# Kernel tuning notes

Measured on AMD Instinct MI355X. Metric: run time of the kernel, lower is better.

## Reference

```python
import jax, jax.numpy as jnp
import numpy as np

MIN_, MAX_, KSZ, IGNORE_IDX = 10, 10, 3, -255
B, H, W = 256, 256, 256
LI_MAX_ITERS = 64


def setup_inputs() -> dict:
    key = jax.random.key(0)
    x = jax.random.uniform(key, (B, 1, H, W), dtype=jnp.float32)
    return {"x": x}


def _otsu(hist):
    # hist: [256] counts. Returns Otsu threshold (bin value); fg = img > t.
    bins = jnp.arange(256, dtype=jnp.float32)
    w0 = jnp.cumsum(hist)[:-1]
    w1 = hist.sum() - w0
    s0 = jnp.cumsum(hist * bins)[:-1]
    s_tot = (hist * bins).sum()
    m0 = s0 / jnp.maximum(w0, 1e-12)
    m1 = (s_tot - s0) / jnp.maximum(w1, 1e-12)
    var_b = w0 * w1 * (m0 - m1) ** 2
    return jnp.argmax(var_b).astype(jnp.float32)


def _li(hist, init_t):
    # Histogram-based Li iterative minimum cross-entropy threshold
    # (skimage.filters.threshold_li with initial_guess=init_t).
    bins = jnp.arange(256, dtype=jnp.float32)
    img_min = jnp.min(jnp.where(hist > 0, bins, 255.0))
    vals = bins - img_min  # shift so values >= 0 (as skimage does)
    csum = jnp.cumsum(hist)
    cvsum = jnp.cumsum(hist * vals)
    n_tot, s_tot = csum[-1], cvsum[-1]
    tol = 0.5  # integer image -> half the minimal value spacing

    def body(state):
        t_curr, _, i = state
        # background: img <= t_curr + img_min
        idx = jnp.clip(jnp.floor(t_curr + img_min).astype(jnp.int32), 0, 255)
        n_back, s_back = csum[idx], cvsum[idx]
        n_fore, s_fore = n_tot - n_back, s_tot - s_back
        mean_back = jnp.where(n_back > 0, s_back / jnp.maximum(n_back, 1.0), 0.0)
        mean_fore = s_fore / jnp.maximum(n_fore, 1.0)
        eps = 1e-12
        t_next = (mean_back - mean_fore) / (
            jnp.log(jnp.maximum(mean_back, eps)) - jnp.log(jnp.maximum(mean_fore, eps)))
        t_next = jnp.where(mean_back < eps, mean_fore / 2.0, t_next)
        return (t_next, t_curr, i + 1)

    def cond(state):
        t_curr, t_prev, i = state
        return (jnp.abs(t_curr - t_prev) > tol) & (i < LI_MAX_ITERS)

    t0 = init_t - img_min
    t_fin, _, _ = jax.lax.while_loop(cond, body, (t0, t0 + 10.0, 0))
    return t_fin + img_min


def _sample_mask(key, region, k):
    # Uniform sampling without replacement of up to k pixels from region
    # (bool [H,W]) via random-score top-k (equiv. to torch.multinomial
    # with uniform probs, w/o replacement).
    flat = region.reshape(-1)
    scores = jnp.where(flat, jax.random.uniform(key, (flat.shape[0],)), -1.0)
    top, idx = jax.lax.top_k(scores, k)
    valid = (top >= 0.0).astype(jnp.int32)
    mask = jnp.zeros(flat.shape[0], jnp.int32).at[idx].max(valid)
    return mask.reshape(region.shape)


def _dilate(m):
    # kornia dilation with ones (KSZ,KSZ) kernel on a 0/1 mask == max filter.
    return jax.lax.reduce_window(m, 0, jax.lax.max, (KSZ, KSZ), (1, 1), "SAME")


def _per_image(img_u8, key_fg, key_bg):
    # img_u8: [H,W] int32 in [0,255]
    hist = jnp.zeros(256, jnp.float32).at[img_u8.ravel()].add(1.0)
    otsu = jnp.clip(_otsu(hist), 1.0, 254.0)  # clamp 0->1, 255->254
    li_t = _li(hist, otsu)
    roi = img_u8.astype(jnp.float32) > li_t

    fg = _sample_mask(key_fg, roi, MAX_)
    bg = _sample_mask(key_bg, jnp.logical_not(roi), MIN_)
    if KSZ > 1:
        fg = _dilate(fg)
        bg = _dilate(bg)

    overlap = (fg + bg) == 2
    fg = jnp.where(overlap, 0, fg)
    bg = jnp.where(overlap, 0, bg)

    seeds = jnp.full((H, W), IGNORE_IDX, jnp.int32)
    seeds = jnp.where(bg == 1, 0, seeds)
    seeds = jnp.where(fg == 1, 1, seeds)
    return seeds


def reference(x):
    b = x.shape[0]
    # (cam*255).astype(uint8): truncation, cam in [0,1]
    img = jnp.clip(jnp.floor(x[:, 0] * 255.0), 0, 255).astype(jnp.int32)
    keys = jax.random.split(jax.random.key(1), (b, 2))
    return jax.vmap(_per_image)(img, keys[:, 0], keys[:, 1])
```

## Files before the change

### kernel.cpp

```cpp
#include <hip/hip_runtime.h>
#include <stdint.h>

#define NPIX 65536
#define IGN (-255)
#define CAP 1022
#define U8N    16384
#define HPART  16384
#define M_THR  18432
#define M_CF   18433
#define M_CB   18434
#define M_NROI 18435
#define M_FG   18436
#define M_BG   19458
#define SCR_I4 5120

__device__ __forceinline__ uint32_t rotl32(uint32_t v, uint32_t r){ return (v<<r)|(v>>(32u-r)); }

__device__ __forceinline__ void tf2x32(uint32_t k0, uint32_t k1, uint32_t x0, uint32_t x1,
                                       uint32_t &o0, uint32_t &o1){
  uint32_t k2 = k0 ^ k1 ^ 0x1BD11BDAu;
  x0 += k0; x1 += k1;
#define TFR(r) { x0 += x1; x1 = rotl32(x1,(r)); x1 ^= x0; }
  TFR(13u) TFR(15u) TFR(26u) TFR(6u)   x0 += k1; x1 += k2 + 1u;
  TFR(17u) TFR(29u) TFR(16u) TFR(24u)  x0 += k2; x1 += k0 + 2u;
  TFR(13u) TFR(15u) TFR(26u) TFR(6u)   x0 += k0; x1 += k1 + 3u;
  TFR(17u) TFR(29u) TFR(16u) TFR(24u)  x0 += k1; x1 += k2 + 4u;
  TFR(13u) TFR(15u) TFR(26u) TFR(6u)   x0 += k2; x1 += k0 + 5u;
#undef TFR
  o0 = x0; o1 = x1;
}

__device__ __forceinline__ unsigned long long packCand(uint32_t bits, uint32_t pix){
  float f = __uint_as_float((bits >> 9) | 0x3f800000u) - 1.0f;
  uint32_t u = __float_as_uint(f) ^ 0x80000000u;
  return ((unsigned long long)u << 32) | (unsigned long long)(0xFFFFFFFFu - pix);
}

__device__ __forceinline__ void t10_insert(unsigned long long* l, unsigned long long c){
  if (c > l[9]) {
    l[9] = c;
#pragma unroll
    for (int i = 9; i > 0; --i){
      unsigned long long a = l[i-1], b2 = l[i];
      if (b2 > a){ l[i-1] = b2; l[i] = a; }
    }
  }
}

__global__ __launch_bounds__(256, 8)
void ka_hist_fill(const float* __restrict__ x, int* __restrict__ out){
  const int blk = blockIdx.x;
  const int b = blk >> 3, j8 = blk & 7;
  const int tid = threadIdx.x;
  const float4* x4 = (const float4*)(x + (size_t)b * NPIX);
  int* base = out + (size_t)b * NPIX;
  int4* o4 = (int4*)base;

  __shared__ uint32_t histR[1024];
#pragma unroll
  for (int k = 0; k < 4; ++k) histR[tid + 256*k] = 0u;
  __syncthreads();

  const int4 f4 = make_int4(IGN, IGN, IGN, IGN);
  const uint32_t c4 = (uint32_t)(tid & 3);
#pragma unroll
  for (int jj = 0; jj < 8; ++jj){
    int i4 = j8*2048 + jj*256 + tid;
    float4 v = x4[i4];
    uint32_t u0 = (uint32_t)min(max((int)floorf(v.x*255.0f),0),255);
    uint32_t u1 = (uint32_t)min(max((int)floorf(v.y*255.0f),0),255);
    uint32_t u2 = (uint32_t)min(max((int)floorf(v.z*255.0f),0),255);
    uint32_t u3 = (uint32_t)min(max((int)floorf(v.w*255.0f),0),255);
    base[i4] = (int)(u0 | (u1<<8) | (u2<<16) | (u3<<24));
    if (i4 >= SCR_I4) o4[i4] = f4;
    atomicAdd(&histR[(u0<<2)|c4],1u); atomicAdd(&histR[(u1<<2)|c4],1u);
    atomicAdd(&histR[(u2<<2)|c4],1u); atomicAdd(&histR[(u3<<2)|c4],1u);
  }
  __syncthreads();
  uint32_t s = histR[4*tid] + histR[4*tid+1] + histR[4*tid+2] + histR[4*tid+3];
  base[HPART + j8*256 + tid] = (int)s;
}

__global__ __launch_bounds__(256, 2)
void kb_thresh(int* __restrict__ out){
  const int b = blockIdx.x;
  const int tid = threadIdx.x;
  int* meta = out + (size_t)b * NPIX;

  __shared__ float csum[256], cvsum[256];
  __shared__ int s_imin;
  __shared__ unsigned long long s_best;
  if (tid == 0){ s_imin = 255; s_best = 0ull; }
  __syncthreads();

  int h = 0;
#pragma unroll
  for (int j = 0; j < 8; ++j) h += meta[HPART + j*256 + tid];
  if (h) atomicMin(&s_imin, tid);
  __syncthreads();
  const float img_min = (float)s_imin;

  csum[tid]  = (float)h;
  cvsum[tid] = (float)h * ((float)tid - img_min);
  __syncthreads();
  for (int off = 1; off < 256; off <<= 1){
    float a = 0.f, c2 = 0.f;
    if (tid >= off){ a = csum[tid-off]; c2 = cvsum[tid-off]; }
    __syncthreads();
    if (tid >= off){ csum[tid] += a; cvsum[tid] += c2; }
    __syncthreads();
  }

  {
    float s_tot_o = cvsum[255] + img_min * csum[255];
    if (tid < 255){
      float w0 = csum[tid];
      float w1 = 65536.0f - w0;
      float cs = cvsum[tid] + img_min * csum[tid];
      float m0 = cs / fmaxf(w0, 1e-12f);
      float m1 = (s_tot_o - cs) / fmaxf(w1, 1e-12f);
      float d = m0 - m1;
      float vb = (w0*w1) * (d*d);
      unsigned long long pk =
        ((unsigned long long)__float_as_uint(vb) << 32) | (unsigned long long)(255 - tid);
      atomicMax(&s_best, pk);
    }
  }
  __syncthreads();

  if (tid == 0){
    int bestIdx = 255 - (int)(s_best & 0xFFFFFFFFull);
    float otsu = fminf(fmaxf((float)bestIdx, 1.0f), 254.0f);
    float n_tot = csum[255], s_tot = cvsum[255];
    float t_curr = otsu - img_min, t_prev = t_curr + 10.0f;
    int it = 0;
    while (fabsf(t_curr - t_prev) > 0.5f && it < 64){
      int idx = min(max((int)floorf(t_curr + img_min), 0), 255);
      float n_back = csum[idx], s_back = cvsum[idx];
      float n_fore = n_tot - n_back, s_fore = s_tot - s_back;
      float mean_back = (n_back > 0.0f) ? (s_back / fmaxf(n_back, 1.0f)) : 0.0f;
      float mean_fore = s_fore / fmaxf(n_fore, 1.0f);
      float t_next = (mean_back - mean_fore) /
                     (logf(fmaxf(mean_back, 1e-12f)) - logf(fmaxf(mean_fore, 1e-12f)));
      if (mean_back < 1e-12f) t_next = mean_fore * 0.5f;
      t_prev = t_curr; t_curr = t_next; ++it;
    }
    float lit = t_curr + img_min;
    int qthr;
    if (!(lit == lit)) qthr = 256;
    else               qthr = (int)floorf(lit) + 1;
    meta[M_THR] = qthr;
    int nlo = (qthr <= 0) ? 0 : (int)csum[min(qthr, 256) - 1];
    meta[M_NROI] = NPIX - nlo;
    meta[M_CF] = 0;
    meta[M_CB] = 0;
  }
}

__global__ __launch_bounds__(256, 8)
void kc_score(int* __restrict__ out){
  const int blk = blockIdx.x;
  const int b = blk >> 3, j8 = blk & 7;
  const int tid = threadIdx.x;
  int* meta = out + (size_t)b * NPIX;
  const int4* u4 = (const int4*)meta;

  __shared__ uint32_t s_kw[4];
  __shared__ int s_thr;
  if (tid < 2){
    uint32_t o0, o1;
    tf2x32(0u, 1u, 0u, (uint32_t)(2*b + tid), o0, o1);
    s_kw[2*tid] = o0; s_kw[2*tid+1] = o1;
  }
  if (tid == 0) s_thr = meta[M_THR];
  __syncthreads();

  const int qthr = s_thr;
  const uint32_t fk0 = s_kw[0], fk1 = s_kw[1], bk0 = s_kw[2], bk1 = s_kw[3];
  const uint32_t THRM = (0xFF000000u >> 9);
  int4 w0 = u4[j8*512 + tid];
  int4 w1 = u4[j8*512 + 256 + tid];
  const uint32_t pixA = (uint32_t)(j8*8192 + 16*tid);
  const uint32_t pixB = (uint32_t)(j8*8192 + 4096 + 16*tid);
#pragma unroll
  for (int half = 0; half < 2; ++half){
    int4 w = half ? w1 : w0;
    uint32_t pb = half ? pixB : pixA;
    const uint32_t words[4] = {(uint32_t)w.x,(uint32_t)w.y,(uint32_t)w.z,(uint32_t)w.w};
#pragma unroll
    for (int m = 0; m < 4; ++m){
      uint32_t pk = words[m];
#pragma unroll
      for (int s = 0; s < 4; ++s){
        int q = (int)((pk >> (8*s)) & 255u);
        bool r = (q >= qthr);
        uint32_t pix = pb + (uint32_t)(4*m + s);
        uint32_t o0, o1;
        tf2x32(r ? fk0 : bk0, r ? fk1 : bk1, 0u, pix, o0, o1);
        uint32_t bits = o0 ^ o1;
        if ((bits >> 9) >= THRM){
          int r2 = r ? 0 : 1;
          int idx = atomicAdd(&meta[M_CF + r2], 1);
          if (idx < CAP) meta[(r2 ? M_BG : M_FG) + idx] = (int)pix;
        }
      }
    }
  }
}

__global__ __launch_bounds__(1024, 4)
void kd_final(int* __restrict__ out){
  const int b = blockIdx.x;
  const int tid = threadIdx.x;
  int* meta = out + (size_t)b * NPIX;
  int* outb = meta;

  __shared__ unsigned long long buf[2][CAP];
  __shared__ uint32_t s_kw[4];
  __shared__ int s_cnt[2], s_fail[2], s_np[2];
  __shared__ int s_thr;
  __shared__ int s_pr[2][10], s_pc[2][10];

  if (tid < 2){
    uint32_t o0, o1;
    tf2x32(0u, 1u, 0u, (uint32_t)(2*b + tid), o0, o1);
    s_kw[2*tid] = o0; s_kw[2*tid+1] = o1;
  }
  if (tid == 0){
    s_thr = meta[M_THR];
    int c0 = meta[M_CF], c1 = meta[M_CB];
    int nroi = meta[M_NROI];
    s_cnt[0] = c0; s_cnt[1] = c1;
    int m0r = nroi, m1r = NPIX - nroi;
    s_fail[0] = (c0 > CAP) || (c0 < 10 && c0 != m0r);
    s_fail[1] = (c1 > CAP) || (c1 < 10 && c1 != m1r);
  }
  __syncthreads();

  {
    int r2 = tid >> 9, lane = tid & 511;
    uint32_t kk0 = s_kw[2*r2], kk1 = s_kw[2*r2+1];
    int n = min(s_cnt[r2], CAP);
    for (int i = lane; i < n; i += 512){
      uint32_t pix = (uint32_t)meta[(r2 ? M_BG : M_FG) + i];
      uint32_t o0, o1; tf2x32(kk0, kk1, 0u, pix, o0, o1);
      buf[r2][i] = packCand(o0 ^ o1, pix);
    }
  }
  __syncthreads();

  const int qthr = s_thr;
  if (s_fail[0] || s_fail[1]){
    if (tid < 64){
      for (int r2 = 0; r2 < 2; ++r2){
        if (!s_fail[r2]) continue;
        uint32_t kk0 = s_kw[2*r2], kk1 = s_kw[2*r2+1];
        unsigned long long t[10];
#pragma unroll
        for (int i = 0; i < 10; ++i) t[i] = 0ull;
        for (int k2 = 0; k2 < 1024; ++k2){
          uint32_t pix = (uint32_t)(tid + 64*k2);
          int q = (int)(((uint32_t)meta[pix >> 2] >> (8*(pix & 3u))) & 255u);
          bool r = (q >= qthr);
          if (r != (r2 == 0)) continue;
          uint32_t o0, o1; tf2x32(kk0, kk1, 0u, pix, o0, o1);
          t10_insert(t, packCand(o0 ^ o1, pix));
        }
#pragma unroll
        for (int i = 0; i < 10; ++i) buf[r2][tid*10 + i] = t[i];
      }
    }
    __syncthreads();
    if (tid < 2 && s_fail[tid]){
      unsigned long long t[10];
#pragma unroll
      for (int i = 0; i < 10; ++i) t[i] = 0ull;
      for (int i = 0; i < 640; ++i) t10_insert(t, buf[tid][i]);
#pragma unroll
      for (int i = 0; i < 10; ++i) buf[tid][i] = t[i];
      s_cnt[tid] = 10;
    }
    __syncthreads();
  }

  if (tid == 0 || tid == 64){
    int r2 = (tid == 0) ? 0 : 1;
    int n = min(s_cnt[r2], CAP);
    unsigned long long t[10];
#pragma unroll
    for (int i = 0; i < 10; ++i) t[i] = 0ull;
    for (int i = 0; i < n; ++i) t10_insert(t, buf[r2][i]);
    int np = 0;
    for (int i = 0; i < 10; ++i){
      if (t[i]){
        uint32_t pix = 0xFFFFFFFFu - (uint32_t)(t[i] & 0xFFFFFFFFull);
        s_pr[r2][np] = (int)(pix >> 8);
        s_pc[r2][np] = (int)(pix & 255u);
        ++np;
      }
    }
    s_np[r2] = np;
  }
  __syncthreads();

#pragma unroll
  for (int k = 0; k < 5; ++k)
    ((int4*)meta)[tid*5 + k] = make_int4(IGN, IGN, IGN, IGN);
  __syncthreads();

  const int nfg = s_np[0], nbg = s_np[1];
  const int npts = nfg + nbg;
  if (tid < npts*9){
    int k = tid / 9, d = tid - k*9;
    int pr = (k < nfg) ? s_pr[0][k] : s_pr[1][k - nfg];
    int pc = (k < nfg) ? s_pc[0][k] : s_pc[1][k - nfg];
    pr += d/3 - 1; pc += d%3 - 1;
    if (pr >= 0 && pr < 256 && pc >= 0 && pc < 256){
      bool fgd = false, bgd = false;
      for (int i = 0; i < nfg; ++i) fgd |= (abs(pr - s_pr[0][i]) <= 1) && (abs(pc - s_pc[0][i]) <= 1);
      for (int i = 0; i < nbg; ++i) bgd |= (abs(pr - s_pr[1][i]) <= 1) && (abs(pc - s_pc[1][i]) <= 1);
      int val = (fgd && bgd) ? IGN : (fgd ? 1 : 0);
      outb[pr*256 + pc] = val;
    }
  }
}

extern "C" void kernel_launch(void* const* d_in, const int* in_sizes, int n_in,
                              void* d_out, int out_size, void* d_ws, size_t ws_size,
                              hipStream_t stream) {
  const float* x = (const float*)d_in[0];
  int* out = (int*)d_out;
  int B = in_sizes[0] / NPIX;
  ka_hist_fill<<<8*B, 256, 0, stream>>>(x, out);
  kb_thresh  <<<B,   256, 0, stream>>>(out);
  kc_score   <<<8*B, 256, 0, stream>>>(out);
  kd_final   <<<B,  1024, 0, stream>>>(out);
}
```

Measured before the change: 196.6 us.

## Fuse threshold into score kernel, aggregate candidates in LDS, shrink final kernel

The per-image threshold computation is folded into the scoring kernel, so each of the 8 blocks per image recomputes the histogram scan and Li iteration redundantly. This drops one kernel launch and its dependency barrier. Candidate pixels are first collected in shared memory and appended to the global list with one atomic per block instead of one global atomic per hit. The final kernel drops from 1024 to 256 threads and does a tree-structured top-10 reduction over wavefronts, which trades redundant threshold work for fewer launches and less global atomic contention.

```diff
diff --git a/kernel.cpp b/kernel.cpp
--- a/kernel.cpp
+++ b/kernel.cpp
@@ -3,15 +3,15 @@
 
 #define NPIX 65536
 #define IGN (-255)
-#define CAP 1022
-#define U8N    16384
+#define CAP 768
+#define LCAP 192
 #define HPART  16384
-#define M_THR  18432
-#define M_CF   18433
-#define M_CB   18434
+#define M_CF   18432
+#define M_CB   18433
+#define M_THR  18434
 #define M_NROI 18435
 #define M_FG   18436
-#define M_BG   19458
+#define M_BG   19204
 #define SCR_I4 5120
 
 __device__ __forceinline__ uint32_t rotl32(uint32_t v, uint32_t r){ return (v<<r)|(v>>(32u-r)); }
@@ -48,7 +48,7 @@
 }
 
 __global__ __launch_bounds__(256, 8)
-void ka_hist_fill(const float* __restrict__ x, int* __restrict__ out){
+void k1_hist_fill(const float* __restrict__ x, int* __restrict__ out){
   const int blk = blockIdx.x;
   const int b = blk >> 3, j8 = blk & 7;
   const int tid = threadIdx.x;
@@ -59,6 +59,7 @@
   __shared__ uint32_t histR[1024];
 #pragma unroll
   for (int k = 0; k < 4; ++k) histR[tid + 256*k] = 0u;
+  if (j8 == 0 && tid == 0){ base[M_CF] = 0; base[M_CB] = 0; }
   __syncthreads();
 
   const int4 f4 = make_int4(IGN, IGN, IGN, IGN);
@@ -81,16 +82,26 @@
   base[HPART + j8*256 + tid] = (int)s;
 }
 
-__global__ __launch_bounds__(256, 2)
-void kb_thresh(int* __restrict__ out){
-  const int b = blockIdx.x;
+__global__ __launch_bounds__(256, 8)
+void k2_score(int* __restrict__ out){
+  const int blk = blockIdx.x;
+  const int b = blk >> 3, j8 = blk & 7;
   const int tid = threadIdx.x;
   int* meta = out + (size_t)b * NPIX;
 
   __shared__ float csum[256], cvsum[256];
-  __shared__ int s_imin;
+  __shared__ int s_imin, s_qthr;
   __shared__ unsigned long long s_best;
-  if (tid == 0){ s_imin = 255; s_best = 0ull; }
+  __shared__ uint32_t s_kw[4];
+  __shared__ int s_lcnt[2], s_base[2];
+  __shared__ int s_lbuf[2][LCAP];
+
+  if (tid == 0){ s_imin = 255; s_best = 0ull; s_lcnt[0] = 0; s_lcnt[1] = 0; }
+  if (tid < 2){
+    uint32_t o0, o1;
+    tf2x32(0u, 1u, 0u, (uint32_t)(2*b + tid), o0, o1);
+    s_kw[2*tid] = o0; s_kw[2*tid+1] = o1;
+  }
   __syncthreads();
 
   int h = 0;
@@ -110,7 +121,6 @@
     if (tid >= off){ csum[tid] += a; cvsum[tid] += c2; }
     __syncthreads();
   }
-
   {
     float s_tot_o = cvsum[255] + img_min * csum[255];
     if (tid < 255){
@@ -127,7 +137,6 @@
     }
   }
   __syncthreads();
-
   if (tid == 0){
     int bestIdx = 255 - (int)(s_best & 0xFFFFFFFFull);
     float otsu = fminf(fmaxf((float)bestIdx, 1.0f), 254.0f);
@@ -149,39 +158,22 @@
     int qthr;
     if (!(lit == lit)) qthr = 256;
     else               qthr = (int)floorf(lit) + 1;
-    meta[M_THR] = qthr;
-    int nlo = (qthr <= 0) ? 0 : (int)csum[min(qthr, 256) - 1];
-    meta[M_NROI] = NPIX - nlo;
-    meta[M_CF] = 0;
-    meta[M_CB] = 0;
-  }
-}
-
-__global__ __launch_bounds__(256, 8)
-void kc_score(int* __restrict__ out){
-  const int blk = blockIdx.x;
-  const int b = blk >> 3, j8 = blk & 7;
-  const int tid = threadIdx.x;
-  int* meta = out + (size_t)b * NPIX;
+    s_qthr = qthr;
+    if (j8 == 0){
+      meta[M_THR] = qthr;
+      int nlo = (qthr <= 0) ? 0 : (int)csum[min(qthr, 256) - 1];
+      meta[M_NROI] = NPIX - nlo;
+    }
+  }
+  __syncthreads();
+
+  const int qthr = s_qthr;
+  const uint32_t fk0 = s_kw[0], fk1 = s_kw[1], bk0 = s_kw[2], bk1 = s_kw[3];
   const int4* u4 = (const int4*)meta;
-
-  __shared__ uint32_t s_kw[4];
-  __shared__ int s_thr;
-  if (tid < 2){
-    uint32_t o0, o1;
-    tf2x32(0u, 1u, 0u, (uint32_t)(2*b + tid), o0, o1);
-    s_kw[2*tid] = o0; s_kw[2*tid+1] = o1;
-  }
-  if (tid == 0) s_thr = meta[M_THR];
-  __syncthreads();
-
-  const int qthr = s_thr;
-  const uint32_t fk0 = s_kw[0], fk1 = s_kw[1], bk0 = s_kw[2], bk1 = s_kw[3];
-  const uint32_t THRM = (0xFF000000u >> 9);
   int4 w0 = u4[j8*512 + tid];
   int4 w1 = u4[j8*512 + 256 + tid];
   const uint32_t pixA = (uint32_t)(j8*8192 + 16*tid);
-  const uint32_t pixB = (uint32_t)(j8*8192 + 4096 + 16*tid);
+  const uint32_t pixB = pixA + 4096u;
 #pragma unroll
   for (int half = 0; half < 2; ++half){
     int4 w = half ? w1 : w0;
@@ -198,27 +190,44 @@
         uint32_t o0, o1;
         tf2x32(r ? fk0 : bk0, r ? fk1 : bk1, 0u, pix, o0, o1);
         uint32_t bits = o0 ^ o1;
-        if ((bits >> 9) >= THRM){
+        if (bits >= 0xFF000000u){
           int r2 = r ? 0 : 1;
-          int idx = atomicAdd(&meta[M_CF + r2], 1);
-          if (idx < CAP) meta[(r2 ? M_BG : M_FG) + idx] = (int)pix;
+          int idx = atomicAdd(&s_lcnt[r2], 1);
+          if (idx < LCAP) s_lbuf[r2][idx] = (int)pix;
         }
       }
     }
   }
-}
-
-__global__ __launch_bounds__(1024, 4)
-void kd_final(int* __restrict__ out){
+  __syncthreads();
+  if (tid < 2){
+    int n = s_lcnt[tid];
+    int add = (n > LCAP) ? (n + CAP + 1) : n;
+    s_base[tid] = atomicAdd(&meta[M_CF + tid], add);
+  }
+  __syncthreads();
+#pragma unroll
+  for (int r2 = 0; r2 < 2; ++r2){
+    int n = min(s_lcnt[r2], LCAP);
+    int bse = s_base[r2];
+    for (int i = tid; i < n; i += 256){
+      int g = bse + i;
+      if (g < CAP) meta[(r2 ? M_BG : M_FG) + g] = s_lbuf[r2][i];
+    }
+  }
+}
+
+__global__ __launch_bounds__(256, 4)
+void k3_final(int* __restrict__ out){
   const int b = blockIdx.x;
   const int tid = threadIdx.x;
   int* meta = out + (size_t)b * NPIX;
   int* outb = meta;
 
-  __shared__ unsigned long long buf[2][CAP];
+  __shared__ unsigned long long s_top[2][64][10];
+  __shared__ unsigned long long s_top2[2][8][10];
   __shared__ uint32_t s_kw[4];
   __shared__ int s_cnt[2], s_fail[2], s_np[2];
-  __shared__ int s_thr;
+  __shared__ int s_qthr;
   __shared__ int s_pr[2][10], s_pc[2][10];
 
   if (tid < 2){
@@ -227,85 +236,80 @@
     s_kw[2*tid] = o0; s_kw[2*tid+1] = o1;
   }
   if (tid == 0){
-    s_thr = meta[M_THR];
+    s_qthr = meta[M_THR];
+    int nroi = meta[M_NROI];
     int c0 = meta[M_CF], c1 = meta[M_CB];
-    int nroi = meta[M_NROI];
     s_cnt[0] = c0; s_cnt[1] = c1;
-    int m0r = nroi, m1r = NPIX - nroi;
-    s_fail[0] = (c0 > CAP) || (c0 < 10 && c0 != m0r);
-    s_fail[1] = (c1 > CAP) || (c1 < 10 && c1 != m1r);
-  }
-  __syncthreads();
-
-  {
-    int r2 = tid >> 9, lane = tid & 511;
-    uint32_t kk0 = s_kw[2*r2], kk1 = s_kw[2*r2+1];
-    int n = min(s_cnt[r2], CAP);
-    for (int i = lane; i < n; i += 512){
-      uint32_t pix = (uint32_t)meta[(r2 ? M_BG : M_FG) + i];
-      uint32_t o0, o1; tf2x32(kk0, kk1, 0u, pix, o0, o1);
-      buf[r2][i] = packCand(o0 ^ o1, pix);
-    }
-  }
-  __syncthreads();
-
-  const int qthr = s_thr;
-  if (s_fail[0] || s_fail[1]){
-    if (tid < 64){
-      for (int r2 = 0; r2 < 2; ++r2){
-        if (!s_fail[r2]) continue;
-        uint32_t kk0 = s_kw[2*r2], kk1 = s_kw[2*r2+1];
-        unsigned long long t[10];
-#pragma unroll
-        for (int i = 0; i < 10; ++i) t[i] = 0ull;
-        for (int k2 = 0; k2 < 1024; ++k2){
-          uint32_t pix = (uint32_t)(tid + 64*k2);
-          int q = (int)(((uint32_t)meta[pix >> 2] >> (8*(pix & 3u))) & 255u);
-          bool r = (q >= qthr);
-          if (r != (r2 == 0)) continue;
+    s_fail[0] = (c0 > CAP) || (c0 < 10 && c0 != nroi);
+    s_fail[1] = (c1 > CAP) || (c1 < 10 && c1 != NPIX - nroi);
+  }
+  __syncthreads();
+
+  const int wv = tid >> 6, lane = tid & 63;
+  if (wv < 2){
+    const int r2 = wv;
+    unsigned long long t[10];
+#pragma unroll
+    for (int i = 0; i < 10; ++i) t[i] = 0ull;
+    const uint32_t kk0 = s_kw[2*r2], kk1 = s_kw[2*r2+1];
+    if (!s_fail[r2]){
+      int n = min(s_cnt[r2], CAP);
+      for (int i = lane; i < n; i += 64){
+        uint32_t pix = (uint32_t)meta[(r2 ? M_BG : M_FG) + i];
+        uint32_t o0, o1; tf2x32(kk0, kk1, 0u, pix, o0, o1);
+        t10_insert(t, packCand(o0 ^ o1, pix));
+      }
+    } else {
+      const int qthr = s_qthr;
+      for (int k = 0; k < 1024; ++k){
+        uint32_t pix = (uint32_t)(lane + 64*k);
+        int q = (int)(((uint32_t)meta[pix >> 2] >> (8*(pix & 3u))) & 255u);
+        bool r = (q >= qthr);
+        if (r == (r2 == 0)){
           uint32_t o0, o1; tf2x32(kk0, kk1, 0u, pix, o0, o1);
           t10_insert(t, packCand(o0 ^ o1, pix));
         }
-#pragma unroll
-        for (int i = 0; i < 10; ++i) buf[r2][tid*10 + i] = t[i];
       }
     }
-    __syncthreads();
-    if (tid < 2 && s_fail[tid]){
-      unsigned long long t[10];
-#pragma unroll
-      for (int i = 0; i < 10; ++i) t[i] = 0ull;
-      for (int i = 0; i < 640; ++i) t10_insert(t, buf[tid][i]);
-#pragma unroll
-      for (int i = 0; i < 10; ++i) buf[tid][i] = t[i];
-      s_cnt[tid] = 10;
-    }
-    __syncthreads();
-  }
-
-  if (tid == 0 || tid == 64){
-    int r2 = (tid == 0) ? 0 : 1;
-    int n = min(s_cnt[r2], CAP);
+#pragma unroll
+    for (int i = 0; i < 10; ++i) s_top[r2][lane][i] = t[i];
+  }
+  __syncthreads();
+  if (wv < 2 && lane < 8){
     unsigned long long t[10];
 #pragma unroll
     for (int i = 0; i < 10; ++i) t[i] = 0ull;
-    for (int i = 0; i < n; ++i) t10_insert(t, buf[r2][i]);
+    for (int l2 = 0; l2 < 8; ++l2)
+#pragma unroll
+      for (int i = 0; i < 10; ++i) t10_insert(t, s_top[wv][lane*8 + l2][i]);
+#pragma unroll
+    for (int i = 0; i < 10; ++i) s_top2[wv][lane][i] = t[i];
+  }
+  __syncthreads();
+  if (wv < 2 && lane == 0){
+    unsigned long long t[10];
+#pragma unroll
+    for (int i = 0; i < 10; ++i) t[i] = 0ull;
+    for (int l2 = 0; l2 < 8; ++l2)
+#pragma unroll
+      for (int i = 0; i < 10; ++i) t10_insert(t, s_top2[wv][l2][i]);
     int np = 0;
     for (int i = 0; i < 10; ++i){
       if (t[i]){
         uint32_t pix = 0xFFFFFFFFu - (uint32_t)(t[i] & 0xFFFFFFFFull);
-        s_pr[r2][np] = (int)(pix >> 8);
-        s_pc[r2][np] = (int)(pix & 255u);
+        s_pr[wv][np] = (int)(pix >> 8);
+        s_pc[wv][np] = (int)(pix & 255u);
         ++np;
       }
     }
-    s_np[r2] = np;
-  }
-  __syncthreads();
-
-#pragma unroll
-  for (int k = 0; k < 5; ++k)
-    ((int4*)meta)[tid*5 + k] = make_int4(IGN, IGN, IGN, IGN);
+    s_np[wv] = np;
+  }
+  __syncthreads();
+
+  const int4 f4 = make_int4(IGN, IGN, IGN, IGN);
+#pragma unroll
+  for (int k = 0; k < 20; ++k)
+    ((int4*)meta)[tid + 256*k] = f4;
   __syncthreads();
 
   const int nfg = s_np[0], nbg = s_np[1];
@@ -331,8 +335,7 @@
   const float* x = (const float*)d_in[0];
   int* out = (int*)d_out;
   int B = in_sizes[0] / NPIX;
-  ka_hist_fill<<<8*B, 256, 0, stream>>>(x, out);
-  kb_thresh  <<<B,   256, 0, stream>>>(out);
-  kc_score   <<<8*B, 256, 0, stream>>>(out);
-  kd_final   <<<B,  1024, 0, stream>>>(out);
-}
+  k1_hist_fill<<<8*B, 256, 0, stream>>>(x, out);
+  k2_score    <<<8*B, 256, 0, stream>>>(out);
+  k3_final    <<<B,   256, 0, stream>>>(out);
+}
```

New measurement: 200.8 us. +2.1%, slower.
